# Performance work log

Hardware: AMD Instinct MI355X
Metric: run time of the kernel (lower is better)

Reference implementation:

```python
import jax, jax.numpy as jnp
import numpy as np

C = 128        # channels
NHEADS = 8
B = 16
HW = 128       # image side; must satisfy HW*HW == C**2 for the module's final view


def setup_inputs() -> dict:
    key = jax.random.key(0)
    k0, k1, k2, k3, k4 = jax.random.split(key, 5)
    x = jax.random.normal(k0, (B, C, HW, HW), jnp.float32)
    w_qkv = jax.random.normal(k1, (3 * C, C), jnp.float32) * 0.02  # 1x1 conv == dense over channel dim
    b_qkv = jax.random.normal(k2, (3 * C,), jnp.float32) * 0.02
    w_out = jax.random.normal(k3, (C, C), jnp.float32) * 0.02
    b_out = jax.random.normal(k4, (C,), jnp.float32) * 0.02
    return {"x": x, "w_qkv": w_qkv, "b_qkv": b_qkv, "w_out": w_out, "b_out": b_out}


def reference(x, w_qkv, b_qkv, w_out, b_out):
    Bx, Cx, Hs, Ws = x.shape
    d = Cx // NHEADS
    N = Hs * Ws  # flattened spatial tokens
    # QKV 1x1 conv (bias=True)
    qkv = jnp.einsum('oc,bchw->bohw', w_qkv, x) + b_qkv[None, :, None, None]
    q, k, v = jnp.split(qkv, 3, axis=1)          # each (B, C, H, W)
    q = q.reshape(Bx, NHEADS, d, N)
    k = k.reshape(Bx, NHEADS, d, N)
    v = v.reshape(Bx, NHEADS, d, N)
    # scaled dot-product attention over the head-channel dim (d x d scores)
    scores = jnp.einsum('bhdn,bhen->bhde', q, k) / jnp.sqrt(jnp.float32(Cx))
    attn = jax.nn.softmax(scores, axis=-1)
    out = jnp.einsum('bhde,bhen->bhdn', attn, v)  # (B, H, d, N)
    side = N // Cx  # module reshapes to (B, C, N//C, N//C); valid since N == C^2
    out = out.reshape(Bx, Cx, side, side)
    # output 1x1 conv
    return jnp.einsum('oc,bchw->bohw', w_out, out) + b_out[None, :, None, None]
```

## Files before the change

### kernel.cpp

```cpp
#include <hip/hip_runtime.h>
#include <math.h>

#define BB 16
#define CC 128
#define NN 16384
#define NHEADS 8
#define HD 16
#define SCALE 0.08838834764831843f

typedef __attribute__((ext_vector_type(8))) short short8;
typedef __attribute__((ext_vector_type(4))) unsigned short ushort4v;
typedef __attribute__((ext_vector_type(16))) float f32x16;

#define CVT(comp, hh, ll)                                                    \
    {                                                                        \
        unsigned int u = __float_as_uint(comp);                              \
        hh = (unsigned short)(u >> 16);                                      \
        float lf = (comp) - __uint_as_float(u & 0xffff0000u);                \
        ll = (unsigned short)(__float_as_uint(lf) >> 16);                    \
    }

__global__ __launch_bounds__(256) void k1_gram(const float* __restrict__ x,
                                               float* __restrict__ pG,
                                               float* __restrict__ pS,
                                               int CH) {
    const int chunk = blockIdx.x;
    const int b = blockIdx.y;
    const int tid = threadIdx.x;
    const int w = tid >> 6;
    const int l = tid & 63;
    const int ch0 = tid >> 4;
    const int t4 = tid & 15;
    const int NCB = NN / CH;
    const int NSTAGE = NCB >> 6;

    __shared__ __align__(16) unsigned short lds[2][2][128 * 64];

    const float* xg = x + (size_t)b * CC * NN + (size_t)chunk * NCB;

    f32x16 acc[10];
#pragma unroll
    for (int t = 0; t < 10; ++t)
#pragma unroll
        for (int r = 0; r < 16; ++r) acc[t][r] = 0.0f;

    float csum[8];
#pragma unroll
    for (int k = 0; k < 8; ++k) csum[k] = 0.0f;

    float4 ld[8];

    auto LOAD = [&](int s) {
#pragma unroll
        for (int k = 0; k < 8; ++k)
            ld[k] = *(const float4*)(xg + (size_t)(ch0 + 16 * k) * NN + s * 64 + t4 * 4);
    };

    auto CVW = [&](int buf) {
#pragma unroll
        for (int k = 0; k < 8; ++k) {
            float4 v = ld[k];
            csum[k] += v.x + v.y + v.z + v.w;
            const int ch = ch0 + 16 * k;
            const int idx = ((ch << 6) + (t4 << 2)) ^ ((ch & 7) << 3);
            unsigned short h0, h1, h2, h3, l0, l1, l2, l3;
            CVT(v.x, h0, l0)
            CVT(v.y, h1, l1)
            CVT(v.z, h2, l2)
            CVT(v.w, h3, l3)
            ushort4v hv = {h0, h1, h2, h3};
            ushort4v lv = {l0, l1, l2, l3};
            *(ushort4v*)&lds[buf][0][idx] = hv;
            *(ushort4v*)&lds[buf][1][idx] = lv;
        }
    };

    const int lr = l & 31, lh = l >> 5;

    LOAD(0);
    CVW(0);
    __syncthreads();

    for (int s = 0; s < NSTAGE; ++s) {
        const int bsel = s & 1;
        if (s + 1 < NSTAGE) LOAD(s + 1);

        short8 fh[4], fl[4];
        const int tb = w * 16 + lh * 8;
#pragma unroll
        for (int cb = 0; cb < 4; ++cb) {
            const int ch = cb * 32 + lr;
            const int idx = ((ch << 6) + tb) ^ ((ch & 7) << 3);
            fh[cb] = *(const short8*)&lds[bsel][0][idx];
            fl[cb] = *(const short8*)&lds[bsel][1][idx];
        }

#define TILE(t, bi, bj)                                                                      \
        acc[t] = __builtin_amdgcn_mfma_f32_32x32x16_bf16(fh[bi], fh[bj], acc[t], 0, 0, 0);   \
        acc[t] = __builtin_amdgcn_mfma_f32_32x32x16_bf16(fh[bi], fl[bj], acc[t], 0, 0, 0);   \
        acc[t] = __builtin_amdgcn_mfma_f32_32x32x16_bf16(fl[bi], fh[bj], acc[t], 0, 0, 0);
        TILE(0, 0, 0) TILE(1, 0, 1) TILE(2, 0, 2) TILE(3, 0, 3) TILE(4, 1, 1)
        TILE(5, 1, 2) TILE(6, 1, 3) TILE(7, 2, 2) TILE(8, 2, 3) TILE(9, 3, 3)
#undef TILE

        if (s + 1 < NSTAGE) CVW((s + 1) & 1);
        __syncthreads();
    }

    float* scr = (float*)&lds[0][0][0];
#pragma unroll
    for (int k = 0; k < 8; ++k) scr[(ch0 + 16 * k) * 16 + t4] = csum[k];
    __syncthreads();
    if (tid < 128) {
        float s2 = 0.0f;
#pragma unroll
        for (int i = 0; i < 16; ++i) s2 += scr[tid * 16 + i];
        pS[(size_t)(b * CH + chunk) * 128 + tid] = s2;
    }
    __syncthreads();

    float* outp = pG + (size_t)(b * CH + chunk) * 10240;
#pragma unroll
    for (int half = 0; half < 2; ++half) {
        if (w > 0) {
#pragma unroll
            for (int tt = 0; tt < 5; ++tt)
#pragma unroll
                for (int r = 0; r < 16; ++r)
                    scr[((w - 1) * 5 + tt) * 1024 + r * 64 + l] = acc[half * 5 + tt][r];
        }
        __syncthreads();
        if (w == 0) {
#pragma unroll
            for (int tt = 0; tt < 5; ++tt)
#pragma unroll
                for (int r = 0; r < 16; ++r)
                    outp[(half * 5 + tt) * 1024 + r * 64 + l] =
                        acc[half * 5 + tt][r]
                        + scr[(0 * 5 + tt) * 1024 + r * 64 + l]
                        + scr[(1 * 5 + tt) * 1024 + r * 64 + l]
                        + scr[(2 * 5 + tt) * 1024 + r * 64 + l];
        }
        __syncthreads();
    }
}

__global__ __launch_bounds__(256) void k1_reduce(const float* __restrict__ pG,
                                                 const float* __restrict__ pS,
                                                 float* __restrict__ G,
                                                 float* __restrict__ sB,
                                                 int CH) {
    const int sg = blockIdx.x;
    const int b = blockIdx.y;
    const int tid = threadIdx.x;

    if (sg < 40) {
        const int e = sg * 256 + tid;
        const int t = e >> 10;
        const int rl = e & 1023;
        float sum = 0.0f;
        const float* p = pG + (size_t)b * CH * 10240 + e;
        for (int ch = 0; ch < CH; ++ch) sum += p[(size_t)ch * 10240];

        int bi, bj;
        if (t < 4)      { bi = 0; bj = t; }
        else if (t < 7) { bi = 1; bj = t - 3; }
        else if (t < 9) { bi = 2; bj = t - 5; }
        else            { bi = 3; bj = 3; }

        const int reg = rl >> 6, lane = rl & 63;
        const int col = bj * 32 + (lane & 31);
        const int row = bi * 32 + (reg & 3) + 8 * (reg >> 2) + 4 * (lane >> 5);
        G[((size_t)b << 14) + row * CC + col] = sum;
        if (bi != bj) G[((size_t)b << 14) + col * CC + row] = sum;
    } else {
        if (tid < 128) {
            float s2 = 0.0f;
            for (int ch = 0; ch < CH; ++ch) s2 += pS[(size_t)(b * CH + ch) * 128 + tid];
            sB[b * CC + tid] = s2;
        }
    }
}

__global__ __launch_bounds__(256) void k2a_attn(const float* __restrict__ G,
                                                const float* __restrict__ sB,
                                                const float* __restrict__ w_qkv,
                                                const float* __restrict__ b_qkv,
                                                float* __restrict__ attn,
                                                float* __restrict__ cpre) {
    const int h = blockIdx.x;
    const int b = blockIdx.y;
    const int tid = threadIdx.x;

    __shared__ float wq_s[HD][132], wk_s[HD][132], Tq[HD][132];
    __shared__ float qs[HD], ks[HD], bqv[HD], bkv[HD], bvv[HD];
    __shared__ float sc[HD][HD + 1];

    for (int idx = tid; idx < HD * CC; idx += 256) {
        int r = idx >> 7, c = idx & 127;
        wq_s[r][c] = w_qkv[(h * HD + r) * CC + c];
        wk_s[r][c] = w_qkv[(CC + h * HD + r) * CC + c];
    }
    if (tid < HD) {
        bqv[tid] = b_qkv[h * HD + tid];
        bkv[tid] = b_qkv[CC + h * HD + tid];
        bvv[tid] = b_qkv[2 * CC + h * HD + tid];
    }
    __syncthreads();

    if (tid < 32) {
        int i = tid & 15;
        bool isK = tid >= 16;
        float sum = 0.0f;
        for (int c = 0; c < CC; ++c)
            sum += (isK ? wk_s[i][c] : wq_s[i][c]) * sB[b * CC + c];
        if (isK) ks[i] = sum; else qs[i] = sum;
    }

    {
        const int c2 = tid & 127;
        const int dh = tid >> 7;
        float t[8];
#pragma unroll
        for (int j = 0; j < 8; ++j) t[j] = 0.0f;
        const float* Gb = G + ((size_t)b << 14);
        for (int c1 = 0; c1 < CC; ++c1) {
            float g = Gb[c1 * CC + c2];
#pragma unroll
            for (int j = 0; j < 8; ++j) t[j] += wq_s[dh * 8 + j][c1] * g;
        }
        __syncthreads();
#pragma unroll
        for (int j = 0; j < 8; ++j) Tq[dh * 8 + j][c2] = t[j];
    }
    __syncthreads();

    {
        const int dd = tid >> 4, e = tid & 15;
        float sum = 0.0f;
        for (int c2 = 0; c2 < CC; ++c2) sum += Tq[dd][c2] * wk_s[e][c2];
        sum += qs[dd] * bkv[e] + bqv[dd] * ks[e] + (float)NN * bqv[dd] * bkv[e];
        sc[dd][e] = sum * SCALE;
    }
    __syncthreads();

    if (tid < HD) {
        const int dd = tid;
        float mx = -1e30f;
#pragma unroll
        for (int e = 0; e < HD; ++e) mx = fmaxf(mx, sc[dd][e]);
        float ex[HD];
        float den = 0.0f;
#pragma unroll
        for (int e = 0; e < HD; ++e) { ex[e] = __expf(sc[dd][e] - mx); den += ex[e]; }
        float inv = 1.0f / den;
        float cp = 0.0f;
#pragma unroll
        for (int e = 0; e < HD; ++e) {
            float a = ex[e] * inv;
            attn[((size_t)b * NHEADS + h) * HD * HD + dd * HD + e] = a;
            cp += a * bvv[e];
        }
        cpre[b * CC + h * HD + dd] = cp;
    }
}

__global__ __launch_bounds__(256) void k2b_M(const float* __restrict__ attn,
                                             const float* __restrict__ cpre,
                                             const float* __restrict__ w_qkv,
                                             const float* __restrict__ w_out,
                                             const float* __restrict__ b_out,
                                             unsigned short* __restrict__ Mh,
                                             unsigned short* __restrict__ Ml,
                                             float* __restrict__ cvec) {
    const int og = blockIdx.x;
    const int b = blockIdx.y;
    const int tid = threadIdx.x;

    __shared__ float Ph[HD][132];
    __shared__ float wo_s[32][129];
    __shared__ float attn_s[CC][HD];
    __shared__ float cpre_s[CC];

    for (int idx = tid; idx < CC * HD; idx += 256)
        attn_s[idx >> 4][idx & 15] = attn[(size_t)b * CC * HD + idx];
    for (int idx = tid; idx < 32 * CC; idx += 256)
        wo_s[idx >> 7][idx & 127] = w_out[(og * 32 + (idx >> 7)) * CC + (idx & 127)];
    if (tid < CC) cpre_s[tid] = cpre[b * CC + tid];
    __syncthreads();

    const int c = tid & 127;
    const int oh = tid >> 7;
    float m[16];
#pragma unroll
    for (int j = 0; j < 16; ++j) m[j] = 0.0f;

    for (int hh = 0; hh < NHEADS; ++hh) {
        for (int idx = tid; idx < HD * CC; idx += 256) {
            int dd = idx >> 7, cc = idx & 127;
            float s = 0.0f;
#pragma unroll
            for (int e = 0; e < HD; ++e)
                s += attn_s[hh * HD + dd][e] * w_qkv[(2 * CC + hh * HD + e) * CC + cc];
            Ph[dd][cc] = s;
        }
        __syncthreads();
#pragma unroll
        for (int dd = 0; dd < HD; ++dd) {
            float p = Ph[dd][c];
#pragma unroll
            for (int j = 0; j < 16; ++j)
                m[j] += wo_s[oh * 16 + j][hh * HD + dd] * p;
        }
        __syncthreads();
    }

#pragma unroll
    for (int j = 0; j < 16; ++j) {
        const int o = og * 32 + oh * 16 + j;
        unsigned short hh2, ll2;
        CVT(m[j], hh2, ll2)
        Mh[((size_t)b << 14) + o * CC + c] = hh2;
        Ml[((size_t)b << 14) + o * CC + c] = ll2;
    }

    if (tid < 32) {
        float s = 0.0f;
        for (int r = 0; r < CC; ++r) s += wo_s[tid][r] * cpre_s[r];
        cvec[b * CC + og * 32 + tid] = s + b_out[og * 32 + tid];
    }
}

__global__ __launch_bounds__(256) void k3_out(const float* __restrict__ x,
                                              const unsigned short* __restrict__ Mh,
                                              const unsigned short* __restrict__ Ml,
                                              const float* __restrict__ cvec,
                                              float* __restrict__ y) {
    const int chunk = blockIdx.x;
    const int b = blockIdx.y;
    const int tid = threadIdx.x;
    const int w = tid >> 6;
    const int lane = tid & 63;

    __shared__ __align__(16) unsigned short xs[2][2][64 * 128];

    const float* xb = x + (size_t)b * CC * NN + (size_t)chunk * 128;

    short8 Ah[8], Al[8];
    {
        const size_t mbase = ((size_t)b << 14) + (size_t)(32 * w + (lane & 31)) * CC;
#pragma unroll
        for (int ks = 0; ks < 8; ++ks) {
            const size_t off = mbase + 16 * ks + 8 * (lane >> 5);
            Ah[ks] = *(const short8*)&Mh[off];
            Al[ks] = *(const short8*)&Ml[off];
        }
    }

    f32x16 acc[4];
#pragma unroll
    for (int t = 0; t < 4; ++t)
#pragma unroll
        for (int r = 0; r < 16; ++r) acc[t][r] = 0.0f;

    float ldv[8][4];

    auto LOAD = [&](int s) {
#pragma unroll
        for (int k = 0; k < 8; ++k) {
            const int c0 = w * 4 + k * 16;
#pragma unroll
            for (int i = 0; i < 4; ++i)
                ldv[k][i] = xb[(size_t)(c0 + i) * NN + s * 64 + lane];
        }
    };

    auto CVW = [&](int buf) {
#pragma unroll
        for (int k = 0; k < 8; ++k) {
            const int c0 = w * 4 + k * 16;
            const int idx = lane * 128 + (c0 ^ ((lane & 7) << 3));
            ushort4v hv, lv;
#pragma unroll
            for (int i = 0; i < 4; ++i) {
                unsigned short hh, ll;
                CVT(ldv[k][i], hh, ll)
                hv[i] = hh;
                lv[i] = ll;
            }
            *(ushort4v*)&xs[buf][0][idx] = hv;
            *(ushort4v*)&xs[buf][1][idx] = lv;
        }
    };

    LOAD(0);
    CVW(0);
    __syncthreads();

#pragma unroll
    for (int s = 0; s < 2; ++s) {
        if (s == 0) LOAD(1);
#pragma unroll
        for (int nt = 0; nt < 2; ++nt) {
            const int nl = nt * 32 + (lane & 31);
            const int cxor = (nl & 7) << 3;
            const int rowb = nl * 128;
#pragma unroll
            for (int ks = 0; ks < 8; ++ks) {
                const int idx = rowb + ((16 * ks + 8 * (lane >> 5)) ^ cxor);
                short8 bh = *(const short8*)&xs[s][0][idx];
                short8 bl = *(const short8*)&xs[s][1][idx];
                const int t = s * 2 + nt;
                acc[t] = __builtin_amdgcn_mfma_f32_32x32x16_bf16(Ah[ks], bh, acc[t], 0, 0, 0);
                acc[t] = __builtin_amdgcn_mfma_f32_32x32x16_bf16(Ah[ks], bl, acc[t], 0, 0, 0);
                acc[t] = __builtin_amdgcn_mfma_f32_32x32x16_bf16(Al[ks], bh, acc[t], 0, 0, 0);
            }
        }
        if (s == 0) CVW(1);
        __syncthreads();
    }

    float cvv[16];
#pragma unroll
    for (int r = 0; r < 16; ++r)
        cvv[r] = cvec[b * CC + 32 * w + (r & 3) + 8 * (r >> 2) + 4 * (lane >> 5)];

    float* yb = y + (size_t)b * CC * NN + (size_t)chunk * 128;
#pragma unroll
    for (int t = 0; t < 4; ++t) {
        const int n = t * 32 + (lane & 31);
#pragma unroll
        for (int r = 0; r < 16; ++r) {
            const int o = 32 * w + (r & 3) + 8 * (r >> 2) + 4 * (lane >> 5);
            yb[(size_t)o * NN + n] = acc[t][r] + cvv[r];
        }
    }
}

extern "C" void kernel_launch(void* const* d_in, const int* in_sizes, int n_in,
                              void* d_out, int out_size, void* d_ws, size_t ws_size,
                              hipStream_t stream) {
    const float* x     = (const float*)d_in[0];
    const float* w_qkv = (const float*)d_in[1];
    const float* b_qkv = (const float*)d_in[2];
    const float* w_out = (const float*)d_in[3];
    const float* b_out = (const float*)d_in[4];
    float* y = (float*)d_out;

    const size_t szG = (size_t)BB * CC * CC;
    const size_t szS = (size_t)BB * CC;
    const size_t szAttn = (size_t)BB * NHEADS * HD * HD;
    const size_t tail = szG + szS + szAttn + szS + szG + szS;

    int CH = 32;
    while (CH > 1 &&
           ((size_t)CH * BB * 10240 + (size_t)CH * BB * CC + tail) * sizeof(float) > ws_size)
        CH >>= 1;

    float* pG   = (float*)d_ws;
    float* pS   = pG + (size_t)CH * BB * 10240;
    float* G    = pS + (size_t)CH * BB * CC;
    float* sB   = G + szG;
    float* attn = sB + szS;
    float* cpre = attn + szAttn;
    float* Mslab = cpre + szS;
    float* cvec = Mslab + szG;

    unsigned short* Mh = (unsigned short*)Mslab;
    unsigned short* Ml = Mh + (size_t)BB * CC * CC;

    k1_gram<<<dim3(CH, BB), 256, 0, stream>>>(x, pG, pS, CH);
    k1_reduce<<<dim3(41, BB), 256, 0, stream>>>(pG, pS, G, sB, CH);
    k2a_attn<<<dim3(NHEADS, BB), 256, 0, stream>>>(G, sB, w_qkv, b_qkv, attn, cpre);
    k2b_M<<<dim3(4, BB), 256, 0, stream>>>(attn, cpre, w_qkv, w_out, b_out, Mh, Ml, cvec);
    k3_out<<<dim3(128, BB), 256, 0, stream>>>(x, Mh, Ml, cvec, y);
}
```

Before: 347.5 us.

## Restructure Gram, attention-prep and output kernels for more parallelism and reuse

The Gram kernel moves to 512 threads, and each wave now owns two full 32x32 output tiles, so the full 16-tile Gram is computed without symmetry and without the LDS cross-wave reduction. The reduce kernel then drops the mirrored transpose write. k2a stages G in shared memory and k2b stages the V weights in shared memory. k3_out now processes 256 tokens per block across four pipelined stages, with split half-loads overlapped with MFMA and a per-stage epilogue. These changes trade more MFMA work and larger partial-Gram traffic for fewer reductions and syncs, plus better latency hiding in the output pass.

```diff
diff --git a/kernel.cpp b/kernel.cpp
--- a/kernel.cpp
+++ b/kernel.cpp
@@ -20,15 +20,16 @@
         ll = (unsigned short)(__float_as_uint(lf) >> 16);                    \
     }
 
-__global__ __launch_bounds__(256) void k1_gram(const float* __restrict__ x,
-                                               float* __restrict__ pG,
-                                               float* __restrict__ pS,
-                                               int CH) {
+__global__ __launch_bounds__(512, 4) void k1_gram(const float* __restrict__ x,
+                                                  float* __restrict__ pG,
+                                                  float* __restrict__ pS,
+                                                  int CH) {
     const int chunk = blockIdx.x;
     const int b = blockIdx.y;
     const int tid = threadIdx.x;
     const int w = tid >> 6;
     const int l = tid & 63;
+    const int lr = l & 31, lh = l >> 5;
     const int ch0 = tid >> 4;
     const int t4 = tid & 15;
     const int NCB = NN / CH;
@@ -38,30 +39,28 @@
 
     const float* xg = x + (size_t)b * CC * NN + (size_t)chunk * NCB;
 
-    f32x16 acc[10];
-#pragma unroll
-    for (int t = 0; t < 10; ++t)
-#pragma unroll
-        for (int r = 0; r < 16; ++r) acc[t][r] = 0.0f;
-
-    float csum[8];
-#pragma unroll
-    for (int k = 0; k < 8; ++k) csum[k] = 0.0f;
-
-    float4 ld[8];
+    const int bi = w >> 1;
+    const int bj0 = (w & 1) * 2;
+
+    f32x16 a0, a1;
+#pragma unroll
+    for (int r = 0; r < 16; ++r) { a0[r] = 0.0f; a1[r] = 0.0f; }
+
+    float csum[4] = {0.0f, 0.0f, 0.0f, 0.0f};
+    float4 ld[4];
 
     auto LOAD = [&](int s) {
 #pragma unroll
-        for (int k = 0; k < 8; ++k)
-            ld[k] = *(const float4*)(xg + (size_t)(ch0 + 16 * k) * NN + s * 64 + t4 * 4);
+        for (int k = 0; k < 4; ++k)
+            ld[k] = *(const float4*)(xg + (size_t)(ch0 + 32 * k) * NN + s * 64 + t4 * 4);
     };
 
     auto CVW = [&](int buf) {
 #pragma unroll
-        for (int k = 0; k < 8; ++k) {
+        for (int k = 0; k < 4; ++k) {
             float4 v = ld[k];
             csum[k] += v.x + v.y + v.z + v.w;
-            const int ch = ch0 + 16 * k;
+            const int ch = ch0 + 32 * k;
             const int idx = ((ch << 6) + (t4 << 2)) ^ ((ch & 7) << 3);
             unsigned short h0, h1, h2, h3, l0, l1, l2, l3;
             CVT(v.x, h0, l0)
@@ -75,33 +74,38 @@
         }
     };
 
-    const int lr = l & 31, lh = l >> 5;
-
     LOAD(0);
     CVW(0);
     __syncthreads();
+
+    const int chA = bi * 32 + lr;
+    const int chB0 = bj0 * 32 + lr;
+    const int chB1 = chB0 + 32;
+    const int swz = (lr & 7) << 3;
 
     for (int s = 0; s < NSTAGE; ++s) {
         const int bsel = s & 1;
         if (s + 1 < NSTAGE) LOAD(s + 1);
 
-        short8 fh[4], fl[4];
-        const int tb = w * 16 + lh * 8;
-#pragma unroll
-        for (int cb = 0; cb < 4; ++cb) {
-            const int ch = cb * 32 + lr;
-            const int idx = ((ch << 6) + tb) ^ ((ch & 7) << 3);
-            fh[cb] = *(const short8*)&lds[bsel][0][idx];
-            fl[cb] = *(const short8*)&lds[bsel][1][idx];
-        }
-
-#define TILE(t, bi, bj)                                                                      \
-        acc[t] = __builtin_amdgcn_mfma_f32_32x32x16_bf16(fh[bi], fh[bj], acc[t], 0, 0, 0);   \
-        acc[t] = __builtin_amdgcn_mfma_f32_32x32x16_bf16(fh[bi], fl[bj], acc[t], 0, 0, 0);   \
-        acc[t] = __builtin_amdgcn_mfma_f32_32x32x16_bf16(fl[bi], fh[bj], acc[t], 0, 0, 0);
-        TILE(0, 0, 0) TILE(1, 0, 1) TILE(2, 0, 2) TILE(3, 0, 3) TILE(4, 1, 1)
-        TILE(5, 1, 2) TILE(6, 1, 3) TILE(7, 2, 2) TILE(8, 2, 3) TILE(9, 3, 3)
-#undef TILE
+#pragma unroll
+        for (int ks = 0; ks < 4; ++ks) {
+            const int tok = ks * 16 + 8 * lh;
+            const int idxA = ((chA << 6) + tok) ^ swz;
+            const int idxB0 = ((chB0 << 6) + tok) ^ swz;
+            const int idxB1 = ((chB1 << 6) + tok) ^ swz;
+            short8 ah = *(const short8*)&lds[bsel][0][idxA];
+            short8 al = *(const short8*)&lds[bsel][1][idxA];
+            short8 b0h = *(const short8*)&lds[bsel][0][idxB0];
+            short8 b0l = *(const short8*)&lds[bsel][1][idxB0];
+            short8 b1h = *(const short8*)&lds[bsel][0][idxB1];
+            short8 b1l = *(const short8*)&lds[bsel][1][idxB1];
+            a0 = __builtin_amdgcn_mfma_f32_32x32x16_bf16(ah, b0h, a0, 0, 0, 0);
+            a0 = __builtin_amdgcn_mfma_f32_32x32x16_bf16(ah, b0l, a0, 0, 0, 0);
+            a0 = __builtin_amdgcn_mfma_f32_32x32x16_bf16(al, b0h, a0, 0, 0, 0);
+            a1 = __builtin_amdgcn_mfma_f32_32x32x16_bf16(ah, b1h, a1, 0, 0, 0);
+            a1 = __builtin_amdgcn_mfma_f32_32x32x16_bf16(ah, b1l, a1, 0, 0, 0);
+            a1 = __builtin_amdgcn_mfma_f32_32x32x16_bf16(al, b1h, a1, 0, 0, 0);
+        }
 
         if (s + 1 < NSTAGE) CVW((s + 1) & 1);
         __syncthreads();
@@ -109,7 +113,7 @@
 
     float* scr = (float*)&lds[0][0][0];
 #pragma unroll
-    for (int k = 0; k < 8; ++k) scr[(ch0 + 16 * k) * 16 + t4] = csum[k];
+    for (int k = 0; k < 4; ++k) scr[(ch0 + 32 * k) * 16 + t4] = csum[k];
     __syncthreads();
     if (tid < 128) {
         float s2 = 0.0f;
@@ -117,31 +121,12 @@
         for (int i = 0; i < 16; ++i) s2 += scr[tid * 16 + i];
         pS[(size_t)(b * CH + chunk) * 128 + tid] = s2;
     }
-    __syncthreads();
-
-    float* outp = pG + (size_t)(b * CH + chunk) * 10240;
-#pragma unroll
-    for (int half = 0; half < 2; ++half) {
-        if (w > 0) {
-#pragma unroll
-            for (int tt = 0; tt < 5; ++tt)
-#pragma unroll
-                for (int r = 0; r < 16; ++r)
-                    scr[((w - 1) * 5 + tt) * 1024 + r * 64 + l] = acc[half * 5 + tt][r];
-        }
-        __syncthreads();
-        if (w == 0) {
-#pragma unroll
-            for (int tt = 0; tt < 5; ++tt)
-#pragma unroll
-                for (int r = 0; r < 16; ++r)
-                    outp[(half * 5 + tt) * 1024 + r * 64 + l] =
-                        acc[half * 5 + tt][r]
-                        + scr[(0 * 5 + tt) * 1024 + r * 64 + l]
-                        + scr[(1 * 5 + tt) * 1024 + r * 64 + l]
-                        + scr[(2 * 5 + tt) * 1024 + r * 64 + l];
-        }
-        __syncthreads();
+
+    float* outp = pG + (size_t)(b * CH + chunk) * 16384;
+#pragma unroll
+    for (int r = 0; r < 16; ++r) {
+        outp[(2 * w) * 1024 + r * 64 + l] = a0[r];
+        outp[(2 * w + 1) * 1024 + r * 64 + l] = a1[r];
     }
 }
 
@@ -154,25 +139,19 @@
     const int b = blockIdx.y;
     const int tid = threadIdx.x;
 
-    if (sg < 40) {
+    if (sg < 64) {
         const int e = sg * 256 + tid;
         const int t = e >> 10;
         const int rl = e & 1023;
         float sum = 0.0f;
-        const float* p = pG + (size_t)b * CH * 10240 + e;
-        for (int ch = 0; ch < CH; ++ch) sum += p[(size_t)ch * 10240];
-
-        int bi, bj;
-        if (t < 4)      { bi = 0; bj = t; }
-        else if (t < 7) { bi = 1; bj = t - 3; }
-        else if (t < 9) { bi = 2; bj = t - 5; }
-        else            { bi = 3; bj = 3; }
-
+        const float* p = pG + (size_t)b * CH * 16384 + e;
+        for (int ch = 0; ch < CH; ++ch) sum += p[(size_t)ch * 16384];
+
+        const int bi = t >> 2, bj = t & 3;
         const int reg = rl >> 6, lane = rl & 63;
         const int col = bj * 32 + (lane & 31);
         const int row = bi * 32 + (reg & 3) + 8 * (reg >> 2) + 4 * (lane >> 5);
         G[((size_t)b << 14) + row * CC + col] = sum;
-        if (bi != bj) G[((size_t)b << 14) + col * CC + row] = sum;
     } else {
         if (tid < 128) {
             float s2 = 0.0f;
@@ -192,10 +171,17 @@
     const int b = blockIdx.y;
     const int tid = threadIdx.x;
 
+    __shared__ float Gs[CC * CC];
     __shared__ float wq_s[HD][132], wk_s[HD][132], Tq[HD][132];
     __shared__ float qs[HD], ks[HD], bqv[HD], bkv[HD], bvv[HD];
     __shared__ float sc[HD][HD + 1];
 
+    {
+        const float4* Gv = (const float4*)(G + ((size_t)b << 14));
+        float4* Gsv = (float4*)Gs;
+#pragma unroll
+        for (int i = 0; i < 16; ++i) Gsv[tid + 256 * i] = Gv[tid + 256 * i];
+    }
     for (int idx = tid; idx < HD * CC; idx += 256) {
         int r = idx >> 7, c = idx & 127;
         wq_s[r][c] = w_qkv[(h * HD + r) * CC + c];
@@ -223,9 +209,8 @@
         float t[8];
 #pragma unroll
         for (int j = 0; j < 8; ++j) t[j] = 0.0f;
-        const float* Gb = G + ((size_t)b << 14);
         for (int c1 = 0; c1 < CC; ++c1) {
-            float g = Gb[c1 * CC + c2];
+            float g = Gs[c1 * CC + c2];
 #pragma unroll
             for (int j = 0; j < 8; ++j) t[j] += wq_s[dh * 8 + j][c1] * g;
         }
@@ -278,6 +263,7 @@
     const int tid = threadIdx.x;
 
     __shared__ float Ph[HD][132];
+    __shared__ float Vs[HD][132];
     __shared__ float wo_s[32][129];
     __shared__ float attn_s[CC][HD];
     __shared__ float cpre_s[CC];
@@ -296,12 +282,15 @@
     for (int j = 0; j < 16; ++j) m[j] = 0.0f;
 
     for (int hh = 0; hh < NHEADS; ++hh) {
+        for (int idx = tid; idx < HD * CC; idx += 256)
+            Vs[idx >> 7][idx & 127] = w_qkv[(2 * CC + hh * HD + (idx >> 7)) * CC + (idx & 127)];
+        __syncthreads();
         for (int idx = tid; idx < HD * CC; idx += 256) {
             int dd = idx >> 7, cc = idx & 127;
             float s = 0.0f;
 #pragma unroll
             for (int e = 0; e < HD; ++e)
-                s += attn_s[hh * HD + dd][e] * w_qkv[(2 * CC + hh * HD + e) * CC + cc];
+                s += attn_s[hh * HD + dd][e] * Vs[e][cc];
             Ph[dd][cc] = s;
         }
         __syncthreads();
@@ -331,11 +320,11 @@
     }
 }
 
-__global__ __launch_bounds__(256) void k3_out(const float* __restrict__ x,
-                                              const unsigned short* __restrict__ Mh,
-                                              const unsigned short* __restrict__ Ml,
-                                              const float* __restrict__ cvec,
-                                              float* __restrict__ y) {
+__global__ __launch_bounds__(256, 4) void k3_out(const float* __restrict__ x,
+                                                 const unsigned short* __restrict__ Mh,
+                                                 const unsigned short* __restrict__ Ml,
+                                                 const float* __restrict__ cvec,
+                                                 float* __restrict__ y) {
     const int chunk = blockIdx.x;
     const int b = blockIdx.y;
     const int tid = threadIdx.x;
@@ -344,7 +333,7 @@
 
     __shared__ __align__(16) unsigned short xs[2][2][64 * 128];
 
-    const float* xb = x + (size_t)b * CC * NN + (size_t)chunk * 128;
+    const float* xb = x + (size_t)b * CC * NN + (size_t)chunk * 256;
 
     short8 Ah[8], Al[8];
     {
@@ -357,28 +346,27 @@
         }
     }
 
-    f32x16 acc[4];
-#pragma unroll
-    for (int t = 0; t < 4; ++t)
-#pragma unroll
-        for (int r = 0; r < 16; ++r) acc[t][r] = 0.0f;
-
-    float ldv[8][4];
-
-    auto LOAD = [&](int s) {
-#pragma unroll
-        for (int k = 0; k < 8; ++k) {
-            const int c0 = w * 4 + k * 16;
+    float cvv[16];
+#pragma unroll
+    for (int r = 0; r < 16; ++r)
+        cvv[r] = cvec[b * CC + 32 * w + (r & 3) + 8 * (r >> 2) + 4 * (lane >> 5)];
+
+    float ldv[4][4];
+
+    auto LOADH = [&](int s, int hf) {
+#pragma unroll
+        for (int k = 0; k < 4; ++k) {
+            const int c0 = w * 4 + (4 * hf + k) * 16;
 #pragma unroll
             for (int i = 0; i < 4; ++i)
                 ldv[k][i] = xb[(size_t)(c0 + i) * NN + s * 64 + lane];
         }
     };
 
-    auto CVW = [&](int buf) {
-#pragma unroll
-        for (int k = 0; k < 8; ++k) {
-            const int c0 = w * 4 + k * 16;
+    auto CVWH = [&](int buf, int hf) {
+#pragma unroll
+        for (int k = 0; k < 4; ++k) {
+            const int c0 = w * 4 + (4 * hf + k) * 16;
             const int idx = lane * 128 + (c0 ^ ((lane & 7) << 3));
             ushort4v hv, lv;
 #pragma unroll
@@ -393,47 +381,54 @@
         }
     };
 
-    LOAD(0);
-    CVW(0);
-    __syncthreads();
-
-#pragma unroll
-    for (int s = 0; s < 2; ++s) {
-        if (s == 0) LOAD(1);
-#pragma unroll
-        for (int nt = 0; nt < 2; ++nt) {
-            const int nl = nt * 32 + (lane & 31);
-            const int cxor = (nl & 7) << 3;
-            const int rowb = nl * 128;
-#pragma unroll
-            for (int ks = 0; ks < 8; ++ks) {
-                const int idx = rowb + ((16 * ks + 8 * (lane >> 5)) ^ cxor);
-                short8 bh = *(const short8*)&xs[s][0][idx];
-                short8 bl = *(const short8*)&xs[s][1][idx];
-                const int t = s * 2 + nt;
-                acc[t] = __builtin_amdgcn_mfma_f32_32x32x16_bf16(Ah[ks], bh, acc[t], 0, 0, 0);
-                acc[t] = __builtin_amdgcn_mfma_f32_32x32x16_bf16(Ah[ks], bl, acc[t], 0, 0, 0);
-                acc[t] = __builtin_amdgcn_mfma_f32_32x32x16_bf16(Al[ks], bh, acc[t], 0, 0, 0);
-            }
-        }
-        if (s == 0) CVW(1);
-        __syncthreads();
-    }
-
-    float cvv[16];
-#pragma unroll
-    for (int r = 0; r < 16; ++r)
-        cvv[r] = cvec[b * CC + 32 * w + (r & 3) + 8 * (r >> 2) + 4 * (lane >> 5)];
-
-    float* yb = y + (size_t)b * CC * NN + (size_t)chunk * 128;
-#pragma unroll
-    for (int t = 0; t < 4; ++t) {
-        const int n = t * 32 + (lane & 31);
+    LOADH(0, 0); CVWH(0, 0);
+    LOADH(0, 1); CVWH(0, 1);
+    __syncthreads();
+
+    float* yb = y + (size_t)b * CC * NN + (size_t)chunk * 256;
+    const int nl0 = lane & 31;
+    const int cx0 = (nl0 & 7) << 3;
+    const int nl1 = 32 + nl0;
+
+    for (int s = 0; s < 4; ++s) {
+        const int bsel = s & 1;
+        f32x16 a0, a1;
+#pragma unroll
+        for (int r = 0; r < 16; ++r) { a0[r] = 0.0f; a1[r] = 0.0f; }
+
+        if (s < 3) LOADH(s + 1, 0);
+
+#pragma unroll
+        for (int ks = 0; ks < 8; ++ks) {
+            const int idx = nl0 * 128 + ((16 * ks + 8 * (lane >> 5)) ^ cx0);
+            short8 bh = *(const short8*)&xs[bsel][0][idx];
+            short8 bl = *(const short8*)&xs[bsel][1][idx];
+            a0 = __builtin_amdgcn_mfma_f32_32x32x16_bf16(Ah[ks], bh, a0, 0, 0, 0);
+            a0 = __builtin_amdgcn_mfma_f32_32x32x16_bf16(Ah[ks], bl, a0, 0, 0, 0);
+            a0 = __builtin_amdgcn_mfma_f32_32x32x16_bf16(Al[ks], bh, a0, 0, 0, 0);
+        }
+
+        if (s < 3) { CVWH(bsel ^ 1, 0); LOADH(s + 1, 1); }
+
+#pragma unroll
+        for (int ks = 0; ks < 8; ++ks) {
+            const int idx = nl1 * 128 + ((16 * ks + 8 * (lane >> 5)) ^ cx0);
+            short8 bh = *(const short8*)&xs[bsel][0][idx];
+            short8 bl = *(const short8*)&xs[bsel][1][idx];
+            a1 = __builtin_amdgcn_mfma_f32_32x32x16_bf16(Ah[ks], bh, a1, 0, 0, 0);
+            a1 = __builtin_amdgcn_mfma_f32_32x32x16_bf16(Ah[ks], bl, a1, 0, 0, 0);
+            a1 = __builtin_amdgcn_mfma_f32_32x32x16_bf16(Al[ks], bh, a1, 0, 0, 0);
+        }
+
+        if (s < 3) CVWH(bsel ^ 1, 1);
+
 #pragma unroll
         for (int r = 0; r < 16; ++r) {
             const int o = 32 * w + (r & 3) + 8 * (r >> 2) + 4 * (lane >> 5);
-            yb[(size_t)o * NN + n] = acc[t][r] + cvv[r];
-        }
+            yb[(size_t)o * NN + s * 64 + nl0] = a0[r] + cvv[r];
+            yb[(size_t)o * NN + s * 64 + nl1] = a1[r] + cvv[r];
+        }
+        __syncthreads();
     }
 }
 
@@ -454,11 +449,11 @@
 
     int CH = 32;
     while (CH > 1 &&
-           ((size_t)CH * BB * 10240 + (size_t)CH * BB * CC + tail) * sizeof(float) > ws_size)
+           ((size_t)CH * BB * 16384 + (size_t)CH * BB * CC + tail) * sizeof(float) > ws_size)
         CH >>= 1;
 
     float* pG   = (float*)d_ws;
-    float* pS   = pG + (size_t)CH * BB * 10240;
+    float* pS   = pG + (size_t)CH * BB * 16384;
     float* G    = pS + (size_t)CH * BB * CC;
     float* sB   = G + szG;
     float* attn = sB + szS;
@@ -469,9 +464,9 @@
     unsigned short* Mh = (unsigned short*)Mslab;
     unsigned short* Ml = Mh + (size_t)BB * CC * CC;
 
-    k1_gram<<<dim3(CH, BB), 256, 0, stream>>>(x, pG, pS, CH);
-    k1_reduce<<<dim3(41, BB), 256, 0, stream>>>(pG, pS, G, sB, CH);
+    k1_gram<<<dim3(CH, BB), 512, 0, stream>>>(x, pG, pS, CH);
+    k1_reduce<<<dim3(65, BB), 256, 0, stream>>>(pG, pS, G, sB, CH);
     k2a_attn<<<dim3(NHEADS, BB), 256, 0, stream>>>(G, sB, w_qkv, b_qkv, attn, cpre);
     k2b_M<<<dim3(4, BB), 256, 0, stream>>>(attn, cpre, w_qkv, w_out, b_out, Mh, Ml, cvec);
-    k3_out<<<dim3(128, BB), 256, 0, stream>>>(x, Mh, Ml, cvec, y);
-}
+    k3_out<<<dim3(64, BB), 256, 0, stream>>>(x, Mh, Ml, cvec, y);
+}
```

After: 348.0 us. About the same (+0.2%).
